# Kernel optimization log

Hardware: AMD Instinct MI355X
Metric: run time of the kernel (lower is better)

The kernel has to match this reference:

```python
import jax, jax.numpy as jnp
import numpy as np

N = 100000
E = 1600000
IN_C = 256
HID = 128
OUT_C = 128
HEADS = 4
C_HEAD = HID // HEADS
BN_EPS = 1e-5
NEG_SLOPE = 0.2


def setup_inputs() -> dict:
    key = jax.random.key(0)
    ks = jax.random.split(key, 12)
    s = lambda fan: 1.0 / np.sqrt(fan)
    return {
        "x": jax.random.normal(ks[0], (N, IN_C), dtype=jnp.float32),
        "W_gat": jax.random.normal(ks[1], (IN_C, HID), dtype=jnp.float32) * s(IN_C),
        "att_src": jax.random.normal(ks[2], (HEADS, C_HEAD), dtype=jnp.float32) * s(C_HEAD),
        "att_dst": jax.random.normal(ks[3], (HEADS, C_HEAD), dtype=jnp.float32) * s(C_HEAD),
        "bias_gat": jnp.zeros((HID,), dtype=jnp.float32),
        "bn1_gamma": jnp.ones((HID,), dtype=jnp.float32),
        "bn1_beta": jnp.zeros((HID,), dtype=jnp.float32),
        "eps_gin": jnp.zeros((), dtype=jnp.float32),
        "lin_W": jax.random.normal(ks[4], (HID, OUT_C), dtype=jnp.float32) * s(HID),
        "lin_b": jnp.zeros((OUT_C,), dtype=jnp.float32),
        "bn2_gamma": jnp.ones((OUT_C,), dtype=jnp.float32),
        "bn2_beta": jnp.zeros((OUT_C,), dtype=jnp.float32),
        "edge_index": jax.random.randint(ks[5], (2, E), 0, N, dtype=jnp.int64),
    }


def batch_norm(h, gamma, beta):
    mu = jnp.mean(h, axis=0)
    var = jnp.var(h, axis=0)
    return (h - mu) * jax.lax.rsqrt(var + BN_EPS) * gamma + beta


def reference(x, W_gat, att_src, att_dst, bias_gat, bn1_gamma, bn1_beta,
              eps_gin, lin_W, lin_b, bn2_gamma, bn2_beta, edge_index):
    src, dst = edge_index[0], edge_index[1]
    # ---- GATConv ----
    h = (x @ W_gat).reshape(N, HEADS, C_HEAD)              # [N,H,C]
    a_src = jnp.einsum('nhc,hc->nh', h, att_src)            # [N,H]
    a_dst = jnp.einsum('nhc,hc->nh', h, att_dst)            # [N,H]
    e = jax.nn.leaky_relu(a_src[src] + a_dst[dst], NEG_SLOPE)  # [E,H]
    # segment softmax over incoming edges of each dst node
    m = jax.ops.segment_max(e, dst, num_segments=N)         # [N,H]
    num = jnp.exp(e - m[dst])                                # [E,H]
    den = jax.ops.segment_sum(num, dst, num_segments=N)      # [N,H]
    alpha = num / den[dst]                                   # [E,H]
    msg = alpha[:, :, None] * h[src]                         # [E,H,C]
    out1 = jax.ops.segment_sum(msg, dst, num_segments=N)     # [N,H,C]
    out1 = out1.reshape(N, HID) + bias_gat
    # BN + ELU (dropout = identity in eval)
    out1 = jax.nn.elu(batch_norm(out1, bn1_gamma, bn1_beta))
    # ---- GINConv: nn((1+eps)*x + sum_neighbors) ----
    agg = jax.ops.segment_sum(out1[src], dst, num_segments=N)
    z = (1.0 + eps_gin) * out1 + agg
    out2 = z @ lin_W + lin_b
    out2 = jax.nn.elu(batch_norm(out2, bn2_gamma, bn2_beta))
    return out2
```

## Files before the change

### kernel.cpp

```cpp
#include <hip/hip_runtime.h>

#define N_NODES 100000
#define N_EDGES 1600000
#define IN_C 256
#define HID 128
#define NEG_SLOPE 0.2f
#define BN_EPS 1e-5f
#define NBUCK 391
#define NPART 391

typedef unsigned int uint32;
typedef __attribute__((ext_vector_type(8))) short bf16x8;
typedef __attribute__((ext_vector_type(4))) float f32x4;

__device__ __forceinline__ float lrelu(float x) { return x > 0.f ? x : NEG_SLOPE * x; }

__device__ __forceinline__ unsigned short f2bf(float f) {
    uint32 u = __float_as_uint(f);
    u += 0x7fffu + ((u >> 16) & 1u);
    return (unsigned short)(u >> 16);
}
__device__ __forceinline__ float bf2f(unsigned short h) {
    return __uint_as_float(((uint32)h) << 16);
}
__device__ __forceinline__ float bflo(uint32 v) { return __uint_as_float(v << 16); }
__device__ __forceinline__ float bfhi(uint32 v) { return __uint_as_float(v & 0xffff0000u); }
__device__ __forceinline__ uint32 packbf(float a, float b) {
    return (uint32)f2bf(a) | ((uint32)f2bf(b) << 16);
}

__global__ void k_init(int* __restrict__ bcount, float* __restrict__ bnacc) {
    int t = threadIdx.x;
    if (t < NBUCK) bcount[t] = 0;
    if (t < 512) bnacc[t] = 0.f;
}

__global__ void k_transpose_all(const float* __restrict__ W1, const float* __restrict__ W2,
                                unsigned short* __restrict__ Wt1,
                                unsigned short* __restrict__ Wt2) {
    int idx = blockIdx.x * 256 + threadIdx.x;
    if (idx < IN_C * 128) {
        int k = idx >> 7, n = idx & 127;
        Wt1[n * IN_C + k] = f2bf(W1[idx]);
    } else {
        idx -= IN_C * 128;
        if (idx < HID * 128) {
            int k = idx >> 7, n = idx & 127;
            Wt2[n * HID + k] = f2bf(W2[idx]);
        }
    }
}

template <bool AF32, bool OUTF32>
__global__ __launch_bounds__(256) void k_gemm(const void* __restrict__ Av,
                                              const unsigned short* __restrict__ Wt,
                                              void* __restrict__ Out, int K) {
    __shared__ unsigned short As[128 * 72];
    __shared__ unsigned short Bs[128 * 72];
    const int t = threadIdx.x;
    const int n0 = blockIdx.x * 128;
    const int wv = t >> 6, lane = t & 63;
    const int wy = wv >> 1, wx = wv & 1;
    const int lm = lane & 15, lg = lane >> 4;
    const float* Af = (const float*)Av;
    const unsigned short* Ah = (const unsigned short*)Av;

    f32x4 acc[4][4];
#pragma unroll
    for (int i = 0; i < 4; ++i)
#pragma unroll
        for (int j = 0; j < 4; ++j) acc[i][j] = (f32x4){0.f, 0.f, 0.f, 0.f};

    float4 afp[8];
    uint4 ahp[4];
    uint4 bvp[4];

    if (AF32) {
#pragma unroll
        for (int p = 0; p < 8; ++p) {
            int idx = p * 256 + t, row = idx >> 4, c4 = idx & 15, gn = n0 + row;
            afp[p] = (gn < N_NODES) ? *(const float4*)&Af[(size_t)gn * K + c4 * 4]
                                    : make_float4(0.f, 0.f, 0.f, 0.f);
        }
    } else {
#pragma unroll
        for (int p = 0; p < 4; ++p) {
            int idx = p * 256 + t, row = idx >> 3, c = idx & 7, gn = n0 + row;
            ahp[p] = (gn < N_NODES) ? *(const uint4*)&Ah[(size_t)gn * K + c * 8]
                                    : make_uint4(0, 0, 0, 0);
        }
    }
#pragma unroll
    for (int p = 0; p < 4; ++p) {
        int idx = p * 256 + t, n = idx >> 3, c = idx & 7;
        bvp[p] = *(const uint4*)&Wt[(size_t)n * K + c * 8];
    }

    for (int kc = 0; kc < K; kc += 64) {
        if (AF32) {
#pragma unroll
            for (int p = 0; p < 8; ++p) {
                int idx = p * 256 + t, row = idx >> 4, c4 = idx & 15;
                ushort4 b;
                b.x = f2bf(afp[p].x); b.y = f2bf(afp[p].y);
                b.z = f2bf(afp[p].z); b.w = f2bf(afp[p].w);
                *(ushort4*)&As[row * 72 + c4 * 4] = b;
            }
        } else {
#pragma unroll
            for (int p = 0; p < 4; ++p) {
                int idx = p * 256 + t, row = idx >> 3, c = idx & 7;
                *(uint4*)&As[row * 72 + c * 8] = ahp[p];
            }
        }
#pragma unroll
        for (int p = 0; p < 4; ++p) {
            int idx = p * 256 + t, n = idx >> 3, c = idx & 7;
            *(uint4*)&Bs[n * 72 + c * 8] = bvp[p];
        }
        __syncthreads();
        int kn = kc + 64;
        if (kn < K) {
            if (AF32) {
#pragma unroll
                for (int p = 0; p < 8; ++p) {
                    int idx = p * 256 + t, row = idx >> 4, c4 = idx & 15, gn = n0 + row;
                    afp[p] = (gn < N_NODES) ? *(const float4*)&Af[(size_t)gn * K + kn + c4 * 4]
                                            : make_float4(0.f, 0.f, 0.f, 0.f);
                }
            } else {
#pragma unroll
                for (int p = 0; p < 4; ++p) {
                    int idx = p * 256 + t, row = idx >> 3, c = idx & 7, gn = n0 + row;
                    ahp[p] = (gn < N_NODES) ? *(const uint4*)&Ah[(size_t)gn * K + kn + c * 8]
                                            : make_uint4(0, 0, 0, 0);
                }
            }
#pragma unroll
            for (int p = 0; p < 4; ++p) {
                int idx = p * 256 + t, n = idx >> 3, c = idx & 7;
                bvp[p] = *(const uint4*)&Wt[(size_t)n * K + kn + c * 8];
            }
        }
#pragma unroll
        for (int ks = 0; ks < 2; ++ks) {
            bf16x8 af[4], bfr[4];
#pragma unroll
            for (int i = 0; i < 4; ++i)
                af[i] = *(const bf16x8*)&As[(wy * 64 + i * 16 + lm) * 72 + ks * 32 + lg * 8];
#pragma unroll
            for (int j = 0; j < 4; ++j)
                bfr[j] = *(const bf16x8*)&Bs[(wx * 64 + j * 16 + lm) * 72 + ks * 32 + lg * 8];
#pragma unroll
            for (int i = 0; i < 4; ++i)
#pragma unroll
                for (int j = 0; j < 4; ++j)
                    acc[i][j] = __builtin_amdgcn_mfma_f32_16x16x32_bf16(af[i], bfr[j],
                                                                        acc[i][j], 0, 0, 0);
        }
        __syncthreads();
    }
#pragma unroll
    for (int i = 0; i < 4; ++i) {
#pragma unroll
        for (int r = 0; r < 4; ++r) {
            int row = n0 + wy * 64 + i * 16 + lg * 4 + r;
            if (row < N_NODES) {
#pragma unroll
                for (int j = 0; j < 4; ++j) {
                    int col = wx * 64 + j * 16 + lm;
                    float v = acc[i][j][r];
                    if (OUTF32) ((float*)Out)[(size_t)row * 128 + col] = v;
                    else ((unsigned short*)Out)[(size_t)row * 128 + col] = f2bf(v);
                }
            }
        }
    }
}

__global__ __launch_bounds__(256) void k_att(const unsigned short* __restrict__ hb,
                                             const float* __restrict__ att_s,
                                             const float* __restrict__ att_d,
                                             float* __restrict__ a_src,
                                             float* __restrict__ a_dst) {
    int node = blockIdx.x * 2 + (threadIdx.x >> 7);
    int c = threadIdx.x & 127;
    float hv = bf2f(hb[(size_t)node * 128 + c]);
    float ps = hv * att_s[c];
    float pd = hv * att_d[c];
#pragma unroll
    for (int m = 1; m < 32; m <<= 1) {
        ps += __shfl_xor(ps, m);
        pd += __shfl_xor(pd, m);
    }
    if ((c & 31) == 0) {
        int head = c >> 5;
        a_src[node * 4 + head] = ps;
        a_dst[node * 4 + head] = pd;
    }
}

__global__ __launch_bounds__(256) void k_bucket_count(const int* __restrict__ ei,
                                                      int* __restrict__ bcount) {
    __shared__ int hist[NBUCK];
    for (int i = threadIdx.x; i < NBUCK; i += 256) hist[i] = 0;
    __syncthreads();
    for (int e = blockIdx.x * 256 + threadIdx.x; e < N_EDGES; e += gridDim.x * 256)
        atomicAdd(&hist[ei[N_EDGES + e] >> 8], 1);
    __syncthreads();
    for (int i = threadIdx.x; i < NBUCK; i += 256)
        if (hist[i]) atomicAdd(&bcount[i], hist[i]);
}

__global__ void k_bucket_scan(const int* __restrict__ bcount, int* __restrict__ bucket_base,
                              int* __restrict__ gcursor, int* __restrict__ row_ptr) {
    __shared__ int sh[512];
    int t = threadIdx.x;
    int v0 = (t < NBUCK) ? bcount[t] : 0;
    int val = v0;
    sh[t] = val;
    __syncthreads();
    for (int off = 1; off < 512; off <<= 1) {
        int o = (t >= off) ? sh[t - off] : 0;
        __syncthreads();
        val += o;
        sh[t] = val;
        __syncthreads();
    }
    if (t < NBUCK) {
        int e = val - v0;
        bucket_base[t] = e;
        gcursor[t] = e;
    }
    if (t == 0) {
        bucket_base[NBUCK] = N_EDGES;
        row_ptr[N_NODES] = N_EDGES;
    }
}

__global__ __launch_bounds__(256) void k_partition(const int* __restrict__ ei,
                                                   int* __restrict__ gcursor,
                                                   int* __restrict__ staging) {
    __shared__ int hist[NBUCK];
    __shared__ int base[NBUCK];
    int t = threadIdx.x;
    int e0 = blockIdx.x * 4096;
    for (int i = t; i < NBUCK; i += 256) hist[i] = 0;
    __syncthreads();
    int pk[16], cb[16];
#pragma unroll
    for (int u = 0; u < 16; ++u) {
        int e = e0 + u * 256 + t;
        cb[u] = -1;
        if (e < N_EDGES) {
            int s = ei[e], d = ei[N_EDGES + e];
            int b = d >> 8;
            int r = atomicAdd(&hist[b], 1);
            pk[u] = ((d & 255) << 17) | s;
            cb[u] = (r << 9) | b;
        }
    }
    __syncthreads();
    for (int i = t; i < NBUCK; i += 256)
        if (hist[i]) base[i] = atomicAdd(&gcursor[i], hist[i]);
    __syncthreads();
#pragma unroll
    for (int u = 0; u < 16; ++u) {
        if (cb[u] >= 0) {
            int b = cb[u] & 511, r = cb[u] >> 9;
            staging[base[b] + r] = pk[u];
        }
    }
}

__global__ __launch_bounds__(256) void k_bucket_sort(const int* __restrict__ staging,
                                                     const int* __restrict__ bucket_base,
                                                     int* __restrict__ row_ptr,
                                                     int* __restrict__ sorted_src) {
    __shared__ int hist[256];
    __shared__ int sh[256];
    int t = threadIdx.x, b = blockIdx.x;
    int lo = bucket_base[b], hi = bucket_base[b + 1];
    hist[t] = 0;
    __syncthreads();
    for (int i = lo + t; i < hi; i += 256) atomicAdd(&hist[staging[i] >> 17], 1);
    __syncthreads();
    int v0 = hist[t];
    int val = v0;
    sh[t] = val;
    __syncthreads();
    for (int off = 1; off < 256; off <<= 1) {
        int o = (t >= off) ? sh[t - off] : 0;
        __syncthreads();
        val += o;
        sh[t] = val;
        __syncthreads();
    }
    int excl = val - v0;
    int d = b * 256 + t;
    if (d < N_NODES) row_ptr[d] = lo + excl;
    hist[t] = excl;
    __syncthreads();
    for (int i = lo + t; i < hi; i += 256) {
        int p = staging[i];
        int r = atomicAdd(&hist[p >> 17], 1);
        sorted_src[lo + r] = p & 0x1FFFF;
    }
}

__global__ __launch_bounds__(256) void k_gat_agg(const uint32* __restrict__ h32,
                                                 const float* __restrict__ a_src,
                                                 const float* __restrict__ a_dst,
                                                 const int* __restrict__ row_ptr,
                                                 const int* __restrict__ sorted_src,
                                                 uint32* __restrict__ out1) {
    __shared__ alignas(16) float wbuf[4][4][72];
    int lane = threadIdx.x & 63, wv = threadIdx.x >> 6;
    int hd = lane >> 4;
    int node = blockIdx.x * 4 + wv;
    int start = row_ptr[node];
    int deg = row_ptr[node + 1] - start;
    if (deg == 0) {
        out1[((uint32)node << 6) + lane] = 0u;
        return;
    }
    float4 ad = *(const float4*)&a_dst[node * 4];
    float acc0 = 0.f, acc1 = 0.f, den = 0.f;
    for (int j0 = 0; j0 < deg; j0 += 64) {
        int m = min(64, deg - j0);
        int s = 0;
        float4 w = make_float4(0.f, 0.f, 0.f, 0.f);
        if (lane < m) {
            s = sorted_src[start + j0 + lane];
            float4 as = *(const float4*)&a_src[s * 4];
            w.x = __expf(lrelu(as.x + ad.x));
            w.y = __expf(lrelu(as.y + ad.y));
            w.z = __expf(lrelu(as.z + ad.z));
            w.w = __expf(lrelu(as.w + ad.w));
        }
        wbuf[wv][0][lane] = w.x;
        wbuf[wv][1][lane] = w.y;
        wbuf[wv][2][lane] = w.z;
        wbuf[wv][3][lane] = w.w;
        __builtin_amdgcn_wave_barrier();
        int e0 = 0;
        for (; e0 + 8 <= m; e0 += 8) {
            uint32 hr[8];
#pragma unroll
            for (int k = 0; k < 8; ++k) {
                int ss = __builtin_amdgcn_readlane(s, e0 + k);
                hr[k] = h32[((uint32)ss << 6) + lane];
            }
            float4 w0 = *(const float4*)&wbuf[wv][hd][e0];
            float4 w1 = *(const float4*)&wbuf[wv][hd][e0 + 4];
            float wk[8] = {w0.x, w0.y, w0.z, w0.w, w1.x, w1.y, w1.z, w1.w};
#pragma unroll
            for (int k = 0; k < 8; ++k) {
                den += wk[k];
                acc0 = fmaf(wk[k], bflo(hr[k]), acc0);
                acc1 = fmaf(wk[k], bfhi(hr[k]), acc1);
            }
        }
        for (; e0 < m; ++e0) {
            int ss = __builtin_amdgcn_readlane(s, e0);
            uint32 hv = h32[((uint32)ss << 6) + lane];
            float wk = wbuf[wv][hd][e0];
            den += wk;
            acc0 = fmaf(wk, bflo(hv), acc0);
            acc1 = fmaf(wk, bfhi(hv), acc1);
        }
        __builtin_amdgcn_wave_barrier();
    }
    float rden = 1.f / den;
    out1[((uint32)node << 6) + lane] = packbf(acc0 * rden, acc1 * rden);
}

__global__ __launch_bounds__(256) void k_gin_agg(const uint32* __restrict__ ob,
                                                 const int* __restrict__ row_ptr,
                                                 const int* __restrict__ sorted_src,
                                                 const float* __restrict__ eps_ptr,
                                                 uint32* __restrict__ zb) {
    int lane = threadIdx.x & 63, wv = threadIdx.x >> 6;
    int node = blockIdx.x * 4 + wv;
    int start = row_ptr[node];
    int deg = row_ptr[node + 1] - start;
    float acc0 = 0.f, acc1 = 0.f;
    for (int j0 = 0; j0 < deg; j0 += 64) {
        int m = min(64, deg - j0);
        int s = 0;
        if (lane < m) s = sorted_src[start + j0 + lane];
        int e0 = 0;
        for (; e0 + 8 <= m; e0 += 8) {
            uint32 hr[8];
#pragma unroll
            for (int k = 0; k < 8; ++k) {
                int ss = __builtin_amdgcn_readlane(s, e0 + k);
                hr[k] = ob[((uint32)ss << 6) + lane];
            }
#pragma unroll
            for (int k = 0; k < 8; ++k) {
                acc0 += bflo(hr[k]);
                acc1 += bfhi(hr[k]);
            }
        }
        for (; e0 < m; ++e0) {
            int ss = __builtin_amdgcn_readlane(s, e0);
            uint32 hv = ob[((uint32)ss << 6) + lane];
            acc0 += bflo(hv);
            acc1 += bfhi(hv);
        }
    }
    float ep = 1.f + eps_ptr[0];
    uint32 own = ob[((uint32)node << 6) + lane];
    zb[((uint32)node << 6) + lane] = packbf(fmaf(ep, bflo(own), acc0),
                                            fmaf(ep, bfhi(own), acc1));
}

__global__ __launch_bounds__(256) void k_bnstats_bf16(const uint32* __restrict__ buf,
                                                      float* __restrict__ acc) {
    __shared__ float sh[4][64][4];
    int lane = threadIdx.x & 63, grp = threadIdx.x >> 6;
    float s0 = 0.f, s1 = 0.f, q0 = 0.f, q1 = 0.f;
    for (int r = blockIdx.x * 4 + grp; r < N_NODES; r += gridDim.x * 4) {
        uint32 v = buf[(size_t)r * 64 + lane];
        float v0 = bflo(v), v1 = bfhi(v);
        s0 += v0; s1 += v1; q0 += v0 * v0; q1 += v1 * v1;
    }
    sh[grp][lane][0] = s0; sh[grp][lane][1] = s1;
    sh[grp][lane][2] = q0; sh[grp][lane][3] = q1;
    __syncthreads();
    if (grp == 0) {
#pragma unroll
        for (int g = 1; g < 4; ++g) {
            s0 += sh[g][lane][0]; s1 += sh[g][lane][1];
            q0 += sh[g][lane][2]; q1 += sh[g][lane][3];
        }
        int c0 = lane * 2;
        atomicAdd(&acc[c0], s0);
        atomicAdd(&acc[c0 + 1], s1);
        atomicAdd(&acc[128 + c0], q0);
        atomicAdd(&acc[128 + c0 + 1], q1);
    }
}

__global__ __launch_bounds__(256) void k_bn_elu_b16(uint32* __restrict__ buf,
                                                    const float* __restrict__ acc,
                                                    const float* __restrict__ gamma,
                                                    const float* __restrict__ beta) {
    __shared__ float psc[128], psh[128];
    int t = threadIdx.x;
    if (t < 128) {
        float mu = acc[t] * (1.f / N_NODES);
        float var = acc[128 + t] * (1.f / N_NODES) - mu * mu;
        float s = rsqrtf(var + BN_EPS) * gamma[t];
        psc[t] = s;
        psh[t] = beta[t] - mu * s;
    }
    __syncthreads();
    size_t i = (size_t)blockIdx.x * 256 + t;
    if (i >= (size_t)N_NODES * 64) return;
    int c0 = (int)(i & 63) * 2;
    uint32 v = buf[i];
    float r0 = fmaf(bflo(v), psc[c0], psh[c0]);
    float r1 = fmaf(bfhi(v), psc[c0 + 1], psh[c0 + 1]);
    r0 = r0 > 0.f ? r0 : __expf(r0) - 1.f;
    r1 = r1 > 0.f ? r1 : __expf(r1) - 1.f;
    buf[i] = packbf(r0, r1);
}

__global__ __launch_bounds__(256) void k_bn_elu_out(const uint32* __restrict__ in,
                                                    const float* __restrict__ acc,
                                                    const float* __restrict__ gamma,
                                                    const float* __restrict__ beta,
                                                    float2* __restrict__ out) {
    __shared__ float psc[128], psh[128];
    int t = threadIdx.x;
    if (t < 128) {
        float mu = acc[t] * (1.f / N_NODES);
        float var = acc[128 + t] * (1.f / N_NODES) - mu * mu;
        float s = rsqrtf(var + BN_EPS) * gamma[t];
        psc[t] = s;
        psh[t] = beta[t] - mu * s;
    }
    __syncthreads();
    size_t i = (size_t)blockIdx.x * 256 + t;
    if (i >= (size_t)N_NODES * 64) return;
    int c0 = (int)(i & 63) * 2;
    uint32 v = in[i];
    float r0 = fmaf(bflo(v), psc[c0], psh[c0]);
    float r1 = fmaf(bfhi(v), psc[c0 + 1], psh[c0 + 1]);
    r0 = r0 > 0.f ? r0 : __expf(r0) - 1.f;
    r1 = r1 > 0.f ? r1 : __expf(r1) - 1.f;
    out[i] = make_float2(r0, r1);
}

extern "C" void kernel_launch(void* const* d_in, const int* in_sizes, int n_in,
                              void* d_out, int out_size, void* d_ws, size_t ws_size,
                              hipStream_t stream) {
    (void)in_sizes; (void)n_in; (void)out_size; (void)ws_size;
    const float* x       = (const float*)d_in[0];
    const float* W_gat   = (const float*)d_in[1];
    const float* att_src = (const float*)d_in[2];
    const float* att_dst = (const float*)d_in[3];
    const float* bn1_g   = (const float*)d_in[5];
    const float* bn1_b   = (const float*)d_in[6];
    const float* eps_gin = (const float*)d_in[7];
    const float* lin_W   = (const float*)d_in[8];
    const float* bn2_g   = (const float*)d_in[10];
    const float* bn2_b   = (const float*)d_in[11];
    const int*   ei      = (const int*)d_in[12];
    float* out = (float*)d_out;

    char* w = (char*)d_ws;
    size_t o = 0;
    auto take = [&](size_t b) -> char* {
        char* p = w + o;
        o += (b + 255) & ~(size_t)255;
        return p;
    };
    unsigned short* hb   = (unsigned short*)take((size_t)N_NODES * 128 * 2);
    unsigned short* Wt1  = (unsigned short*)take((size_t)128 * IN_C * 2);
    unsigned short* Wt2  = (unsigned short*)take((size_t)128 * HID * 2);
    uint32* o1b          = (uint32*)take((size_t)N_NODES * 64 * 4);
    float* a_src         = (float*)take((size_t)N_NODES * 4 * 4);
    float* a_dst         = (float*)take((size_t)N_NODES * 4 * 4);
    int*   sorted        = (int*)take((size_t)N_EDGES * 4);
    int*   staging       = (int*)take((size_t)N_EDGES * 4);
    int*   row_ptr       = (int*)take((size_t)(N_NODES + 1) * 4);
    int*   bcount        = (int*)take((NBUCK + 1) * 4);
    int*   bucket_base   = (int*)take((NBUCK + 1) * 4);
    int*   gcursor       = (int*)take((NBUCK + 1) * 4);
    float* bnacc         = (float*)take(512 * 4);
    uint32* zb  = (uint32*)hb;
    uint32* o2b = o1b;

    const int nGemmBlocks = (N_NODES + 127) / 128;
    const int nElemBlocks = (N_NODES * 64 + 255) / 256;

    k_init<<<1, 512, 0, stream>>>(bcount, bnacc);
    k_transpose_all<<<((IN_C + HID) * 128 + 255) / 256, 256, 0, stream>>>(W_gat, lin_W,
                                                                          Wt1, Wt2);
    k_gemm<true, false><<<nGemmBlocks, 256, 0, stream>>>(x, Wt1, hb, IN_C);
    k_att<<<N_NODES / 2, 256, 0, stream>>>(hb, att_src, att_dst, a_src, a_dst);
    k_bucket_count<<<256, 256, 0, stream>>>(ei, bcount);
    k_bucket_scan<<<1, 512, 0, stream>>>(bcount, bucket_base, gcursor, row_ptr);
    k_partition<<<NPART, 256, 0, stream>>>(ei, gcursor, staging);
    k_bucket_sort<<<NBUCK, 256, 0, stream>>>(staging, bucket_base, row_ptr, sorted);
    k_gat_agg<<<N_NODES / 4, 256, 0, stream>>>((const uint32*)hb, a_src, a_dst, row_ptr,
                                               sorted, o1b);
    k_bnstats_bf16<<<512, 256, 0, stream>>>(o1b, bnacc);
    k_bn_elu_b16<<<nElemBlocks, 256, 0, stream>>>(o1b, bnacc, bn1_g, bn1_b);
    k_gin_agg<<<N_NODES / 4, 256, 0, stream>>>(o1b, row_ptr, sorted, eps_gin, zb);
    k_gemm<false, false><<<nGemmBlocks, 256, 0, stream>>>(zb, Wt2, o2b, HID);
    k_bnstats_bf16<<<512, 256, 0, stream>>>(o2b, bnacc + 256);
    k_bn_elu_out<<<nElemBlocks, 256, 0, stream>>>(o2b, bnacc + 256, bn2_g, bn2_b,
                                                  (float2*)out);
}
```

Baseline: 546.3 us.

## Fuse attention logits and BN statistics into GEMM and GAT epilogues

```diff
diff --git a/kernel.cpp b/kernel.cpp
--- a/kernel.cpp
+++ b/kernel.cpp
@@ -8,6 +8,7 @@
 #define BN_EPS 1e-5f
 #define NBUCK 391
 #define NPART 391
+#define GAT_BLOCKS 2048
 
 typedef unsigned int uint32;
 typedef __attribute__((ext_vector_type(8))) short bf16x8;
@@ -51,10 +52,15 @@
     }
 }
 
-template <bool AF32, bool OUTF32>
+template <bool AF32, bool OUTF32, bool ATT, bool STATS>
 __global__ __launch_bounds__(256) void k_gemm(const void* __restrict__ Av,
                                               const unsigned short* __restrict__ Wt,
-                                              void* __restrict__ Out, int K) {
+                                              void* __restrict__ Out, int K,
+                                              const float* __restrict__ att_s,
+                                              const float* __restrict__ att_d,
+                                              float* __restrict__ a_src,
+                                              float* __restrict__ a_dst,
+                                              float* __restrict__ bnst) {
     __shared__ unsigned short As[128 * 72];
     __shared__ unsigned short Bs[128 * 72];
     const int t = threadIdx.x;
@@ -160,43 +166,70 @@
         }
         __syncthreads();
     }
+
+    float as_w[4], ad_w[4];
+    if (ATT) {
+#pragma unroll
+        for (int j = 0; j < 4; ++j) {
+            int col = wx * 64 + j * 16 + lm;
+            as_w[j] = att_s[col];
+            ad_w[j] = att_d[col];
+        }
+    }
+    float ls[4] = {0.f, 0.f, 0.f, 0.f}, lq[4] = {0.f, 0.f, 0.f, 0.f};
 #pragma unroll
     for (int i = 0; i < 4; ++i) {
 #pragma unroll
         for (int r = 0; r < 4; ++r) {
             int row = n0 + wy * 64 + i * 16 + lg * 4 + r;
+            float v0 = acc[i][0][r], v1 = acc[i][1][r];
+            float v2 = acc[i][2][r], v3 = acc[i][3][r];
             if (row < N_NODES) {
-#pragma unroll
-                for (int j = 0; j < 4; ++j) {
-                    int col = wx * 64 + j * 16 + lm;
-                    float v = acc[i][j][r];
-                    if (OUTF32) ((float*)Out)[(size_t)row * 128 + col] = v;
-                    else ((unsigned short*)Out)[(size_t)row * 128 + col] = f2bf(v);
-                }
-            }
-        }
-    }
-}
-
-__global__ __launch_bounds__(256) void k_att(const unsigned short* __restrict__ hb,
-                                             const float* __restrict__ att_s,
-                                             const float* __restrict__ att_d,
-                                             float* __restrict__ a_src,
-                                             float* __restrict__ a_dst) {
-    int node = blockIdx.x * 2 + (threadIdx.x >> 7);
-    int c = threadIdx.x & 127;
-    float hv = bf2f(hb[(size_t)node * 128 + c]);
-    float ps = hv * att_s[c];
-    float pd = hv * att_d[c];
-#pragma unroll
-    for (int m = 1; m < 32; m <<= 1) {
-        ps += __shfl_xor(ps, m);
-        pd += __shfl_xor(pd, m);
-    }
-    if ((c & 31) == 0) {
-        int head = c >> 5;
-        a_src[node * 4 + head] = ps;
-        a_dst[node * 4 + head] = pd;
+                if (OUTF32) {
+                    float* op = (float*)Out + (size_t)row * 128 + wx * 64 + lm;
+                    op[0] = v0; op[16] = v1; op[32] = v2; op[48] = v3;
+                } else {
+                    unsigned short* op =
+                        (unsigned short*)Out + (size_t)row * 128 + wx * 64 + lm;
+                    op[0] = f2bf(v0); op[16] = f2bf(v1);
+                    op[32] = f2bf(v2); op[48] = f2bf(v3);
+                }
+            }
+            if (STATS) {
+                ls[0] += v0; lq[0] += v0 * v0;
+                ls[1] += v1; lq[1] += v1 * v1;
+                ls[2] += v2; lq[2] += v2 * v2;
+                ls[3] += v3; lq[3] += v3 * v3;
+            }
+            if (ATT) {
+                float ps0 = v0 * as_w[0] + v1 * as_w[1];
+                float ps1 = v2 * as_w[2] + v3 * as_w[3];
+                float pd0 = v0 * ad_w[0] + v1 * ad_w[1];
+                float pd1 = v2 * ad_w[2] + v3 * ad_w[3];
+#pragma unroll
+                for (int m = 1; m < 16; m <<= 1) {
+                    ps0 += __shfl_xor(ps0, m); ps1 += __shfl_xor(ps1, m);
+                    pd0 += __shfl_xor(pd0, m); pd1 += __shfl_xor(pd1, m);
+                }
+                if (lm == 0 && row < N_NODES) {
+                    *(float2*)&a_src[row * 4 + wx * 2] = make_float2(ps0, ps1);
+                    *(float2*)&a_dst[row * 4 + wx * 2] = make_float2(pd0, pd1);
+                }
+            }
+        }
+    }
+    if (STATS) {
+#pragma unroll
+        for (int j = 0; j < 4; ++j) {
+            float s = ls[j], q = lq[j];
+            s += __shfl_xor(s, 16); s += __shfl_xor(s, 32);
+            q += __shfl_xor(q, 16); q += __shfl_xor(q, 32);
+            if (lg == 0) {
+                int col = wx * 64 + j * 16 + lm;
+                atomicAdd(&bnst[col], s);
+                atomicAdd(&bnst[128 + col], q);
+            }
+        }
     }
 }
 
@@ -313,66 +346,88 @@
                                                  const float* __restrict__ a_dst,
                                                  const int* __restrict__ row_ptr,
                                                  const int* __restrict__ sorted_src,
-                                                 uint32* __restrict__ out1) {
+                                                 uint32* __restrict__ out1,
+                                                 float* __restrict__ bnacc) {
     __shared__ alignas(16) float wbuf[4][4][72];
+    __shared__ float sred[4][64][4];
     int lane = threadIdx.x & 63, wv = threadIdx.x >> 6;
     int hd = lane >> 4;
-    int node = blockIdx.x * 4 + wv;
-    int start = row_ptr[node];
-    int deg = row_ptr[node + 1] - start;
-    if (deg == 0) {
-        out1[((uint32)node << 6) + lane] = 0u;
-        return;
-    }
-    float4 ad = *(const float4*)&a_dst[node * 4];
-    float acc0 = 0.f, acc1 = 0.f, den = 0.f;
-    for (int j0 = 0; j0 < deg; j0 += 64) {
-        int m = min(64, deg - j0);
-        int s = 0;
-        float4 w = make_float4(0.f, 0.f, 0.f, 0.f);
-        if (lane < m) {
-            s = sorted_src[start + j0 + lane];
-            float4 as = *(const float4*)&a_src[s * 4];
-            w.x = __expf(lrelu(as.x + ad.x));
-            w.y = __expf(lrelu(as.y + ad.y));
-            w.z = __expf(lrelu(as.z + ad.z));
-            w.w = __expf(lrelu(as.w + ad.w));
-        }
-        wbuf[wv][0][lane] = w.x;
-        wbuf[wv][1][lane] = w.y;
-        wbuf[wv][2][lane] = w.z;
-        wbuf[wv][3][lane] = w.w;
-        __builtin_amdgcn_wave_barrier();
-        int e0 = 0;
-        for (; e0 + 8 <= m; e0 += 8) {
-            uint32 hr[8];
-#pragma unroll
-            for (int k = 0; k < 8; ++k) {
-                int ss = __builtin_amdgcn_readlane(s, e0 + k);
-                hr[k] = h32[((uint32)ss << 6) + lane];
-            }
-            float4 w0 = *(const float4*)&wbuf[wv][hd][e0];
-            float4 w1 = *(const float4*)&wbuf[wv][hd][e0 + 4];
-            float wk[8] = {w0.x, w0.y, w0.z, w0.w, w1.x, w1.y, w1.z, w1.w};
-#pragma unroll
-            for (int k = 0; k < 8; ++k) {
-                den += wk[k];
-                acc0 = fmaf(wk[k], bflo(hr[k]), acc0);
-                acc1 = fmaf(wk[k], bfhi(hr[k]), acc1);
-            }
-        }
-        for (; e0 < m; ++e0) {
-            int ss = __builtin_amdgcn_readlane(s, e0);
-            uint32 hv = h32[((uint32)ss << 6) + lane];
-            float wk = wbuf[wv][hd][e0];
-            den += wk;
-            acc0 = fmaf(wk, bflo(hv), acc0);
-            acc1 = fmaf(wk, bfhi(hv), acc1);
-        }
-        __builtin_amdgcn_wave_barrier();
-    }
-    float rden = 1.f / den;
-    out1[((uint32)node << 6) + lane] = packbf(acc0 * rden, acc1 * rden);
+    float s0 = 0.f, s1 = 0.f, q0 = 0.f, q1 = 0.f;
+    for (int node = blockIdx.x * 4 + wv; node < N_NODES; node += GAT_BLOCKS * 4) {
+        int start = row_ptr[node];
+        int deg = row_ptr[node + 1] - start;
+        if (deg == 0) {
+            out1[((uint32)node << 6) + lane] = 0u;
+            continue;
+        }
+        float4 ad = *(const float4*)&a_dst[node * 4];
+        float acc0 = 0.f, acc1 = 0.f, den = 0.f;
+        for (int j0 = 0; j0 < deg; j0 += 64) {
+            int m = min(64, deg - j0);
+            int s = 0;
+            float4 w = make_float4(0.f, 0.f, 0.f, 0.f);
+            if (lane < m) {
+                s = sorted_src[start + j0 + lane];
+                float4 as = *(const float4*)&a_src[s * 4];
+                w.x = __expf(lrelu(as.x + ad.x));
+                w.y = __expf(lrelu(as.y + ad.y));
+                w.z = __expf(lrelu(as.z + ad.z));
+                w.w = __expf(lrelu(as.w + ad.w));
+            }
+            wbuf[wv][0][lane] = w.x;
+            wbuf[wv][1][lane] = w.y;
+            wbuf[wv][2][lane] = w.z;
+            wbuf[wv][3][lane] = w.w;
+            __builtin_amdgcn_wave_barrier();
+            int e0 = 0;
+            for (; e0 + 8 <= m; e0 += 8) {
+                uint32 hr[8];
+#pragma unroll
+                for (int k = 0; k < 8; ++k) {
+                    int ss = __builtin_amdgcn_readlane(s, e0 + k);
+                    hr[k] = h32[((uint32)ss << 6) + lane];
+                }
+                float4 w0 = *(const float4*)&wbuf[wv][hd][e0];
+                float4 w1 = *(const float4*)&wbuf[wv][hd][e0 + 4];
+                float wk[8] = {w0.x, w0.y, w0.z, w0.w, w1.x, w1.y, w1.z, w1.w};
+#pragma unroll
+                for (int k = 0; k < 8; ++k) {
+                    den += wk[k];
+                    acc0 = fmaf(wk[k], bflo(hr[k]), acc0);
+                    acc1 = fmaf(wk[k], bfhi(hr[k]), acc1);
+                }
+            }
+            for (; e0 < m; ++e0) {
+                int ss = __builtin_amdgcn_readlane(s, e0);
+                uint32 hv = h32[((uint32)ss << 6) + lane];
+                float wk = wbuf[wv][hd][e0];
+                den += wk;
+                acc0 = fmaf(wk, bflo(hv), acc0);
+                acc1 = fmaf(wk, bfhi(hv), acc1);
+            }
+            __builtin_amdgcn_wave_barrier();
+        }
+        float rden = 1.f / den;
+        float o0 = acc0 * rden, o1 = acc1 * rden;
+        s0 += o0; q0 += o0 * o0;
+        s1 += o1; q1 += o1 * o1;
+        out1[((uint32)node << 6) + lane] = packbf(o0, o1);
+    }
+    sred[wv][lane][0] = s0; sred[wv][lane][1] = s1;
+    sred[wv][lane][2] = q0; sred[wv][lane][3] = q1;
+    __syncthreads();
+    if (wv == 0) {
+#pragma unroll
+        for (int g = 1; g < 4; ++g) {
+            s0 += sred[g][lane][0]; s1 += sred[g][lane][1];
+            q0 += sred[g][lane][2]; q1 += sred[g][lane][3];
+        }
+        int c0 = lane * 2;
+        atomicAdd(&bnacc[c0], s0);
+        atomicAdd(&bnacc[c0 + 1], s1);
+        atomicAdd(&bnacc[128 + c0], q0);
+        atomicAdd(&bnacc[128 + c0 + 1], q1);
+    }
 }
 
 __global__ __launch_bounds__(256) void k_gin_agg(const uint32* __restrict__ ob,
@@ -414,33 +469,6 @@
     uint32 own = ob[((uint32)node << 6) + lane];
     zb[((uint32)node << 6) + lane] = packbf(fmaf(ep, bflo(own), acc0),
                                             fmaf(ep, bfhi(own), acc1));
-}
-
-__global__ __launch_bounds__(256) void k_bnstats_bf16(const uint32* __restrict__ buf,
-                                                      float* __restrict__ acc) {
-    __shared__ float sh[4][64][4];
-    int lane = threadIdx.x & 63, grp = threadIdx.x >> 6;
-    float s0 = 0.f, s1 = 0.f, q0 = 0.f, q1 = 0.f;
-    for (int r = blockIdx.x * 4 + grp; r < N_NODES; r += gridDim.x * 4) {
-        uint32 v = buf[(size_t)r * 64 + lane];
-        float v0 = bflo(v), v1 = bfhi(v);
-        s0 += v0; s1 += v1; q0 += v0 * v0; q1 += v1 * v1;
-    }
-    sh[grp][lane][0] = s0; sh[grp][lane][1] = s1;
-    sh[grp][lane][2] = q0; sh[grp][lane][3] = q1;
-    __syncthreads();
-    if (grp == 0) {
-#pragma unroll
-        for (int g = 1; g < 4; ++g) {
-            s0 += sh[g][lane][0]; s1 += sh[g][lane][1];
-            q0 += sh[g][lane][2]; q1 += sh[g][lane][3];
-        }
-        int c0 = lane * 2;
-        atomicAdd(&acc[c0], s0);
-        atomicAdd(&acc[c0 + 1], s1);
-        atomicAdd(&acc[128 + c0], q0);
-        atomicAdd(&acc[128 + c0 + 1], q1);
-    }
 }
 
 __global__ __launch_bounds__(256) void k_bn_elu_b16(uint32* __restrict__ buf,
@@ -540,19 +568,18 @@
     k_init<<<1, 512, 0, stream>>>(bcount, bnacc);
     k_transpose_all<<<((IN_C + HID) * 128 + 255) / 256, 256, 0, stream>>>(W_gat, lin_W,
                                                                           Wt1, Wt2);
-    k_gemm<true, false><<<nGemmBlocks, 256, 0, stream>>>(x, Wt1, hb, IN_C);
-    k_att<<<N_NODES / 2, 256, 0, stream>>>(hb, att_src, att_dst, a_src, a_dst);
+    k_gemm<true, false, true, false><<<nGemmBlocks, 256, 0, stream>>>(
+        x, Wt1, hb, IN_C, att_src, att_dst, a_src, a_dst, nullptr);
     k_bucket_count<<<256, 256, 0, stream>>>(ei, bcount);
     k_bucket_scan<<<1, 512, 0, stream>>>(bcount, bucket_base, gcursor, row_ptr);
     k_partition<<<NPART, 256, 0, stream>>>(ei, gcursor, staging);
     k_bucket_sort<<<NBUCK, 256, 0, stream>>>(staging, bucket_base, row_ptr, sorted);
-    k_gat_agg<<<N_NODES / 4, 256, 0, stream>>>((const uint32*)hb, a_src, a_dst, row_ptr,
-                                               sorted, o1b);
-    k_bnstats_bf16<<<512, 256, 0, stream>>>(o1b, bnacc);
+    k_gat_agg<<<GAT_BLOCKS, 256, 0, stream>>>((const uint32*)hb, a_src, a_dst, row_ptr,
+                                              sorted, o1b, bnacc);
     k_bn_elu_b16<<<nElemBlocks, 256, 0, stream>>>(o1b, bnacc, bn1_g, bn1_b);
     k_gin_agg<<<N_NODES / 4, 256, 0, stream>>>(o1b, row_ptr, sorted, eps_gin, zb);
-    k_gemm<false, false><<<nGemmBlocks, 256, 0, stream>>>(zb, Wt2, o2b, HID);
-    k_bnstats_bf16<<<512, 256, 0, stream>>>(o2b, bnacc + 256);
+    k_gemm<false, false, false, true><<<nGemmBlocks, 256, 0, stream>>>(
+        zb, Wt2, o2b, HID, nullptr, nullptr, nullptr, nullptr, bnacc + 256);
     k_bn_elu_out<<<nElemBlocks, 256, 0, stream>>>(o2b, bnacc + 256, bn2_g, bn2_b,
                                                   (float2*)out);
 }
```

Result: slower. 576.9 us (+5.6%).
